# Optimization experiments

Measured on AMD Instinct MI355X. Metric: run time of the kernel, lower is better.

## Reference

```python
import jax, jax.numpy as jnp
import numpy as np

B, SQ, SK, DIM, HEADS, DH = 2, 1024, 1024, 512, 1, 64
INNER = HEADS * DH  # 64


def setup_inputs() -> dict:
    key = jax.random.key(0)
    ks = jax.random.split(key, 7)
    s = 0.05
    return {
        "x": jax.random.normal(ks[0], (B, SQ, DIM), jnp.float32),
        "emb": jax.random.normal(ks[1], (B, SK, DIM), jnp.float32),
        "Wq": jax.random.normal(ks[2], (DIM, INNER), jnp.float32) * s,
        "Wk": jax.random.normal(ks[3], (DIM, INNER), jnp.float32) * s,
        "Wv": jax.random.normal(ks[4], (DIM, INNER), jnp.float32) * s,
        "Wo": jax.random.normal(ks[5], (INNER, DIM), jnp.float32) * s,
        "bo": jnp.zeros((DIM,), jnp.float32),
    }


def reference(x, emb, Wq, Wk, Wv, Wo, bo):
    # QKV projections (bias-free Dense layers)
    q = x @ Wq     # [B, SQ, INNER]
    k = emb @ Wk   # [B, SK, INNER]
    v = emb @ Wv   # [B, SK, INNER]
    # Faithful to the module's reshape: (B, -1, inner_dim, heads).
    # With heads=1 the attention sees num_heads=INNER and q_features=heads=1.
    q = q.reshape(q.shape[0], -1, q.shape[-1], HEADS)  # [B, SQ, INNER, 1]
    k = k.reshape(k.shape[0], -1, k.shape[-1], HEADS)  # [B, SK, INNER, 1]
    v = v.reshape(v.shape[0], -1, v.shape[-1], HEADS)  # [B, SK, INNER, 1]
    # Memory-efficient attention scales q by q_features**-0.5 (here =1)
    scale = jnp.asarray(q.shape[-1], q.dtype) ** -0.5
    s = jnp.einsum('bqhd,bkhd->bqhk', q * scale, k)    # [B, SQ, INNER, SK]
    p = jax.nn.softmax(s, axis=-1)
    o = jnp.einsum('bqhk,bkhd->bqhd', p, v)            # [B, SQ, INNER, 1]
    o = o.reshape(x.shape[0], x.shape[1], -1)          # [B, SQ, INNER]
    return o @ Wo + bo                                 # [B, SQ, DIM]
```

## Files before the change

kernel.cpp:

```cpp
#include <hip/hip_runtime.h>
#include <hip/hip_bf16.h>

#define LOG2E 1.44269504088896340736f

__device__ __forceinline__ float fast_exp2(float x) {
#if __has_builtin(__builtin_amdgcn_exp2f)
    return __builtin_amdgcn_exp2f(x);
#else
    return exp2f(x);
#endif
}

__global__ __launch_bounds__(256) void proj_kernel(
    const float* __restrict__ x, const float* __restrict__ emb,
    const float* __restrict__ Wq, const float* __restrict__ Wk,
    const float* __restrict__ Wv,
    float* __restrict__ qT, float* __restrict__ kT, float* __restrict__ vT)
{
    __shared__ __align__(16) float sx[4096];
    __shared__ __align__(16) float sred[4096];
    const int t   = threadIdx.x;
    const int bid = blockIdx.x;
    const bool isQ = (bid < 256);
    const int rb  = isQ ? bid : (bid - 256);

    const float* src = (isQ ? x : emb) + (size_t)rb * 8 * 512;
    #pragma unroll
    for (int i = 0; i < 16; ++i) sx[i * 256 + t] = src[i * 256 + t];
    __syncthreads();

    const int b  = rb >> 7;
    const int q0 = (rb << 3) & 1023;

    if (isQ) {
        const int cp = (t & 31) * 2;
        const int g  = t >> 5;
        const int d0 = g * 64;
        float acc0[8], acc1[8];
        #pragma unroll
        for (int r = 0; r < 8; ++r) { acc0[r] = 0.f; acc1[r] = 0.f; }
        for (int dd = 0; dd < 64; dd += 4) {
            const int d = d0 + dd;
            float2 w0 = *(const float2*)&Wq[(d + 0) * 64 + cp];
            float2 w1 = *(const float2*)&Wq[(d + 1) * 64 + cp];
            float2 w2 = *(const float2*)&Wq[(d + 2) * 64 + cp];
            float2 w3 = *(const float2*)&Wq[(d + 3) * 64 + cp];
            #pragma unroll
            for (int r = 0; r < 8; ++r) {
                float4 xv = *(const float4*)&sx[r * 512 + d];
                acc0[r] = fmaf(xv.x, w0.x, acc0[r]); acc1[r] = fmaf(xv.x, w0.y, acc1[r]);
                acc0[r] = fmaf(xv.y, w1.x, acc0[r]); acc1[r] = fmaf(xv.y, w1.y, acc1[r]);
                acc0[r] = fmaf(xv.z, w2.x, acc0[r]); acc1[r] = fmaf(xv.z, w2.y, acc1[r]);
                acc0[r] = fmaf(xv.w, w3.x, acc0[r]); acc1[r] = fmaf(xv.w, w3.y, acc1[r]);
            }
        }
        #pragma unroll
        for (int r = 0; r < 8; ++r)
            *(float2*)&sred[g * 512 + r * 64 + cp] = make_float2(acc0[r], acc1[r]);
        __syncthreads();
        #pragma unroll
        for (int p = 0; p < 2; ++p) {
            int idx = p * 256 + t;
            int r = idx >> 6, h = idx & 63;
            float s = 0.f;
            #pragma unroll
            for (int g2 = 0; g2 < 8; ++g2) s += sred[g2 * 512 + r * 64 + h];
            qT[(size_t)(b * 64 + h) * 1024 + q0 + r] = s;
        }
    } else {
        const int cp = (t & 63) * 2;
        const int g  = t >> 6;
        const int d0 = g * 128;
        const float* Wsel = (cp < 64) ? (Wk + cp) : (Wv + (cp - 64));
        float acc0[8], acc1[8];
        #pragma unroll
        for (int r = 0; r < 8; ++r) { acc0[r] = 0.f; acc1[r] = 0.f; }
        for (int dd = 0; dd < 128; dd += 4) {
            const int d = d0 + dd;
            float2 w0 = *(const float2*)&Wsel[(d + 0) * 64];
            float2 w1 = *(const float2*)&Wsel[(d + 1) * 64];
            float2 w2 = *(const float2*)&Wsel[(d + 2) * 64];
            float2 w3 = *(const float2*)&Wsel[(d + 3) * 64];
            #pragma unroll
            for (int r = 0; r < 8; ++r) {
                float4 xv = *(const float4*)&sx[r * 512 + d];
                acc0[r] = fmaf(xv.x, w0.x, acc0[r]); acc1[r] = fmaf(xv.x, w0.y, acc1[r]);
                acc0[r] = fmaf(xv.y, w1.x, acc0[r]); acc1[r] = fmaf(xv.y, w1.y, acc1[r]);
                acc0[r] = fmaf(xv.z, w2.x, acc0[r]); acc1[r] = fmaf(xv.z, w2.y, acc1[r]);
                acc0[r] = fmaf(xv.w, w3.x, acc0[r]); acc1[r] = fmaf(xv.w, w3.y, acc1[r]);
            }
        }
        #pragma unroll
        for (int r = 0; r < 8; ++r)
            *(float2*)&sred[g * 1024 + r * 128 + cp] = make_float2(acc0[r], acc1[r]);
        __syncthreads();
        #pragma unroll
        for (int p = 0; p < 4; ++p) {
            int idx = p * 256 + t;
            int r = idx >> 7, c = idx & 127;
            float s = 0.f;
            #pragma unroll
            for (int g2 = 0; g2 < 4; ++g2) s += sred[g2 * 1024 + r * 128 + c];
            if (c < 64) kT[(size_t)(b * 64 + c) * 1024 + q0 + r] = s;
            else        vT[(size_t)(b * 64 + (c - 64)) * 1024 + q0 + r] = s;
        }
    }
}

__global__ __launch_bounds__(256) void attn_kernel(
    const float* __restrict__ qT, const float* __restrict__ kT,
    const float* __restrict__ vT, float* __restrict__ O)
{
    __shared__ __align__(16) float kc[1024];
    __shared__ __align__(16) float vc[1024];
    __shared__ float wred[8];
    const int t   = threadIdx.x;
    const int bid = blockIdx.x;
    const int b   = bid >> 7;
    const int h   = (bid >> 1) & 63;
    const int qh  = bid & 1;
    const size_t base = (size_t)(b * 64 + h) * 1024;

    float kmx = -1e30f, kmn = 1e30f;
    #pragma unroll
    for (int i = 0; i < 4; ++i) {
        float kv = kT[base + i * 256 + t];
        float vv = vT[base + i * 256 + t];
        kc[i * 256 + t] = kv;
        vc[i * 256 + t] = vv;
        kmx = fmaxf(kmx, kv);
        kmn = fminf(kmn, kv);
    }
    #pragma unroll
    for (int off = 32; off >= 1; off >>= 1) {
        kmx = fmaxf(kmx, __shfl_xor(kmx, off));
        kmn = fminf(kmn, __shfl_xor(kmn, off));
    }
    const int wid = t >> 6;
    if ((t & 63) == 0) { wred[wid] = kmx; wred[4 + wid] = kmn; }
    __syncthreads();
    kmx = fmaxf(fmaxf(wred[0], wred[1]), fmaxf(wred[2], wred[3]));
    kmn = fminf(fminf(wred[4], wred[5]), fminf(wred[6], wred[7]));

    const int qa = qh * 512 + t;
    const int qb = qa + 256;
    const float qsa = qT[base + qa];
    const float qsb = qT[base + qb];
    const float ma  = (qsa >= 0.f) ? qsa * kmx : qsa * kmn;
    const float mb  = (qsb >= 0.f) ? qsb * kmx : qsb * kmn;
    const float aa  = qsa * LOG2E;
    const float ab  = qsb * LOG2E;
    const float ba  = -ma * LOG2E;
    const float bb  = -mb * LOG2E;

    float da0 = 0.f, da1 = 0.f, da2 = 0.f, da3 = 0.f;
    float na0 = 0.f, na1 = 0.f, na2 = 0.f, na3 = 0.f;
    float db0 = 0.f, db1 = 0.f, db2 = 0.f, db3 = 0.f;
    float nb0 = 0.f, nb1 = 0.f, nb2 = 0.f, nb3 = 0.f;
    const float4* kc4 = (const float4*)kc;
    const float4* vc4 = (const float4*)vc;
    for (int j = 0; j < 256; ++j) {
        float4 k4 = kc4[j];
        float4 v4 = vc4[j];
        float ea0 = fast_exp2(fmaf(aa, k4.x, ba));
        float ea1 = fast_exp2(fmaf(aa, k4.y, ba));
        float ea2 = fast_exp2(fmaf(aa, k4.z, ba));
        float ea3 = fast_exp2(fmaf(aa, k4.w, ba));
        float eb0 = fast_exp2(fmaf(ab, k4.x, bb));
        float eb1 = fast_exp2(fmaf(ab, k4.y, bb));
        float eb2 = fast_exp2(fmaf(ab, k4.z, bb));
        float eb3 = fast_exp2(fmaf(ab, k4.w, bb));
        da0 += ea0; na0 = fmaf(ea0, v4.x, na0);
        da1 += ea1; na1 = fmaf(ea1, v4.y, na1);
        da2 += ea2; na2 = fmaf(ea2, v4.z, na2);
        da3 += ea3; na3 = fmaf(ea3, v4.w, na3);
        db0 += eb0; nb0 = fmaf(eb0, v4.x, nb0);
        db1 += eb1; nb1 = fmaf(eb1, v4.y, nb1);
        db2 += eb2; nb2 = fmaf(eb2, v4.z, nb2);
        db3 += eb3; nb3 = fmaf(eb3, v4.w, nb3);
    }
    const float dena = (da0 + da1) + (da2 + da3);
    const float numa = (na0 + na1) + (na2 + na3);
    const float denb = (db0 + db1) + (db2 + db3);
    const float numb = (nb0 + nb1) + (nb2 + nb3);
    O[(size_t)(b * 1024 + qa) * 64 + h] = numa / dena;
    O[(size_t)(b * 1024 + qb) * 64 + h] = numb / denb;
}

__global__ __launch_bounds__(256) void oproj_kernel(
    const float* __restrict__ O, const float* __restrict__ Wo,
    const float* __restrict__ bo, float* __restrict__ out)
{
    __shared__ __align__(16) float so[512];
    const int t  = threadIdx.x;
    const int rb = blockIdx.x;
    const size_t r0 = (size_t)rb * 8;
    so[t]       = O[r0 * 64 + t];
    so[t + 256] = O[r0 * 64 + t + 256];
    __syncthreads();

    const int d2 = t * 2;
    float2 bv = *(const float2*)&bo[d2];
    float acc0[8], acc1[8];
    #pragma unroll
    for (int r = 0; r < 8; ++r) { acc0[r] = bv.x; acc1[r] = bv.y; }
    for (int hh = 0; hh < 64; hh += 4) {
        float2 w0 = *(const float2*)&Wo[(hh + 0) * 512 + d2];
        float2 w1 = *(const float2*)&Wo[(hh + 1) * 512 + d2];
        float2 w2 = *(const float2*)&Wo[(hh + 2) * 512 + d2];
        float2 w3 = *(const float2*)&Wo[(hh + 3) * 512 + d2];
        #pragma unroll
        for (int r = 0; r < 8; ++r) {
            float4 s4 = *(const float4*)&so[r * 64 + hh];
            acc0[r] = fmaf(s4.x, w0.x, acc0[r]); acc1[r] = fmaf(s4.x, w0.y, acc1[r]);
            acc0[r] = fmaf(s4.y, w1.x, acc0[r]); acc1[r] = fmaf(s4.y, w1.y, acc1[r]);
            acc0[r] = fmaf(s4.z, w2.x, acc0[r]); acc1[r] = fmaf(s4.z, w2.y, acc1[r]);
            acc0[r] = fmaf(s4.w, w3.x, acc0[r]); acc1[r] = fmaf(s4.w, w3.y, acc1[r]);
        }
    }
    #pragma unroll
    for (int r = 0; r < 8; ++r)
        *(float2*)&out[(r0 + r) * 512 + d2] = make_float2(acc0[r], acc1[r]);
}

extern "C" void kernel_launch(void* const* d_in, const int* in_sizes, int n_in,
                              void* d_out, int out_size, void* d_ws, size_t ws_size,
                              hipStream_t stream)
{
    const float* x   = (const float*)d_in[0];
    const float* emb = (const float*)d_in[1];
    const float* Wq  = (const float*)d_in[2];
    const float* Wk  = (const float*)d_in[3];
    const float* Wv  = (const float*)d_in[4];
    const float* Wo  = (const float*)d_in[5];
    const float* bo  = (const float*)d_in[6];
    float* out = (float*)d_out;

    float* qT = (float*)d_ws;
    float* kT = qT + 131072;
    float* vT = kT + 131072;
    float* O  = vT + 131072;

    proj_kernel<<<512, 256, 0, stream>>>(x, emb, Wq, Wk, Wv, qT, kT, vT);
    attn_kernel<<<256, 256, 0, stream>>>(qT, kT, vT, O);
    oproj_kernel<<<256, 256, 0, stream>>>(O, Wo, bo, out);
}
```

Measured before the change: 113.3 us.

## Split attention key range across two blocks and merge partials in oproj

The attention kernel now divides the 1024 keys into two halves, one per block, doubling the grid from 256 to 512 blocks. Each block writes partial numerators and denominators, and the output projection kernel sums the two halves and divides before the matmul. This is meant to fill more compute units on the GPU, since 256 blocks underoccupy the device. The cost is extra workspace traffic for the partials and a redundant key min/max scan in every block. Both halves share the same global max bound, so the partials can be added directly.

```diff
diff --git a/kernel.cpp b/kernel.cpp
--- a/kernel.cpp
+++ b/kernel.cpp
@@ -109,28 +109,31 @@
 
 __global__ __launch_bounds__(256) void attn_kernel(
     const float* __restrict__ qT, const float* __restrict__ kT,
-    const float* __restrict__ vT, float* __restrict__ O)
-{
-    __shared__ __align__(16) float kc[1024];
-    __shared__ __align__(16) float vc[1024];
+    const float* __restrict__ vT, float* __restrict__ numP,
+    float* __restrict__ denP)
+{
+    __shared__ __align__(16) float kc[512];
+    __shared__ __align__(16) float vc[512];
     __shared__ float wred[8];
     const int t   = threadIdx.x;
     const int bid = blockIdx.x;
-    const int b   = bid >> 7;
-    const int h   = (bid >> 1) & 63;
-    const int qh  = bid & 1;
+    const int b   = bid >> 8;
+    const int h   = (bid >> 2) & 63;
+    const int qh  = (bid >> 1) & 1;
+    const int jh  = bid & 1;
     const size_t base = (size_t)(b * 64 + h) * 1024;
 
     float kmx = -1e30f, kmn = 1e30f;
     #pragma unroll
     for (int i = 0; i < 4; ++i) {
         float kv = kT[base + i * 256 + t];
-        float vv = vT[base + i * 256 + t];
-        kc[i * 256 + t] = kv;
-        vc[i * 256 + t] = vv;
         kmx = fmaxf(kmx, kv);
         kmn = fminf(kmn, kv);
-    }
+        if ((i >> 1) == jh) kc[(i & 1) * 256 + t] = kv;
+    }
+    #pragma unroll
+    for (int i2 = 0; i2 < 2; ++i2)
+        vc[i2 * 256 + t] = vT[base + (jh * 2 + i2) * 256 + t];
     #pragma unroll
     for (int off = 32; off >= 1; off >>= 1) {
         kmx = fmaxf(kmx, __shfl_xor(kmx, off));
@@ -159,7 +162,7 @@
     float nb0 = 0.f, nb1 = 0.f, nb2 = 0.f, nb3 = 0.f;
     const float4* kc4 = (const float4*)kc;
     const float4* vc4 = (const float4*)vc;
-    for (int j = 0; j < 256; ++j) {
+    for (int j = 0; j < 128; ++j) {
         float4 k4 = kc4[j];
         float4 v4 = vc4[j];
         float ea0 = fast_exp2(fmaf(aa, k4.x, ba));
@@ -183,20 +186,28 @@
     const float numa = (na0 + na1) + (na2 + na3);
     const float denb = (db0 + db1) + (db2 + db3);
     const float numb = (nb0 + nb1) + (nb2 + nb3);
-    O[(size_t)(b * 1024 + qa) * 64 + h] = numa / dena;
-    O[(size_t)(b * 1024 + qb) * 64 + h] = numb / denb;
+    const size_t pa = (size_t)jh * 131072 + (size_t)(b * 1024 + qa) * 64 + h;
+    const size_t pb = (size_t)jh * 131072 + (size_t)(b * 1024 + qb) * 64 + h;
+    numP[pa] = numa; denP[pa] = dena;
+    numP[pb] = numb; denP[pb] = denb;
 }
 
 __global__ __launch_bounds__(256) void oproj_kernel(
-    const float* __restrict__ O, const float* __restrict__ Wo,
-    const float* __restrict__ bo, float* __restrict__ out)
+    const float* __restrict__ numP, const float* __restrict__ denP,
+    const float* __restrict__ Wo, const float* __restrict__ bo,
+    float* __restrict__ out)
 {
     __shared__ __align__(16) float so[512];
     const int t  = threadIdx.x;
     const int rb = blockIdx.x;
     const size_t r0 = (size_t)rb * 8;
-    so[t]       = O[r0 * 64 + t];
-    so[t + 256] = O[r0 * 64 + t + 256];
+    #pragma unroll
+    for (int p = 0; p < 2; ++p) {
+        const size_t gi = r0 * 64 + p * 256 + t;
+        float n = numP[gi] + numP[gi + 131072];
+        float d = denP[gi] + denP[gi + 131072];
+        so[p * 256 + t] = n / d;
+    }
     __syncthreads();
 
     const int d2 = t * 2;
@@ -236,12 +247,13 @@
     const float* bo  = (const float*)d_in[6];
     float* out = (float*)d_out;
 
-    float* qT = (float*)d_ws;
-    float* kT = qT + 131072;
-    float* vT = kT + 131072;
-    float* O  = vT + 131072;
+    float* qT   = (float*)d_ws;
+    float* kT   = qT + 131072;
+    float* vT   = kT + 131072;
+    float* numP = vT + 131072;
+    float* denP = numP + 262144;
 
     proj_kernel<<<512, 256, 0, stream>>>(x, emb, Wq, Wk, Wv, qT, kT, vT);
-    attn_kernel<<<256, 256, 0, stream>>>(qT, kT, vT, O);
-    oproj_kernel<<<256, 256, 0, stream>>>(O, Wo, bo, out);
-}
+    attn_kernel<<<512, 256, 0, stream>>>(qT, kT, vT, numP, denP);
+    oproj_kernel<<<256, 256, 0, stream>>>(numP, denP, Wo, bo, out);
+}
```

Result: faster. 110.2 us (-2.8%).
